# Kernel tuning notes

Measured on AMD Instinct MI355X. Metric: run time of the kernel, lower is better.

The kernel has to match this reference:

```python
import jax, jax.numpy as jnp
import numpy as np

N_ORDER = 256
PRED_LEN = 192
SEQ_LEN = 768
ENC_IN = 21
BATCH = 16
MULTISCALE = [1, 2, 4]
MODES = 32  # min(32, min(pred_len, seq_len)//2)


def _transition(N):
    Q = np.arange(N, dtype=np.float64)
    R = (2 * Q + 1)[:, None]
    j, i = np.meshgrid(Q, Q)
    A = np.where(i < j, -1, (-1.0) ** (i - j + 1)) * R
    B = (-1.0) ** Q[:, None] * R
    return A, B


def _bilinear(A, B, dt):
    # scipy cont2discrete(method='bilinear'): Ad=(I-dt/2 A)^-1 (I+dt/2 A), Bd=(I-dt/2 A)^-1 dt B
    N = A.shape[0]
    I = np.eye(N)
    ima = I - (dt / 2.0) * A
    Ad = np.linalg.solve(ima, I + (dt / 2.0) * A)
    Bd = np.linalg.solve(ima, dt * B)
    return Ad, Bd.squeeze(-1)


def _legendre_eval(N, x):
    # Legendre P_n(x) via three-term recurrence; returns [len(x), N]
    T = x.shape[0]
    P = np.zeros((N, T))
    P[0] = 1.0
    if N > 1:
        P[1] = x
    for n in range(2, N):
        P[n] = ((2 * n - 1) * x * P[n - 1] - (n - 1) * P[n - 2]) / n
    return P.T


def setup_inputs() -> dict:
    key = jax.random.key(0)
    ks = jax.random.split(key, 12)
    inp = {"x_enc": jax.random.normal(ks[0], (BATCH, SEQ_LEN, ENC_IN), dtype=jnp.float32)}
    Ac, Bc = _transition(N_ORDER)
    scale = 1.0 / (N_ORDER * N_ORDER)
    for idx, m in enumerate(MULTISCALE):
        dt = 1.0 / PRED_LEN / m
        Ad, Bd = _bilinear(Ac, Bc, dt)
        vals = np.arange(0.0, 1.0, dt)
        E = _legendre_eval(N_ORDER, 1.0 - 2.0 * vals)
        inp[f"A{idx}"] = jnp.asarray(Ad, jnp.float32)
        inp[f"B{idx}"] = jnp.asarray(Bd, jnp.float32)
        inp[f"E{idx}"] = jnp.asarray(E, jnp.float32)
        inp[f"Wr{idx}"] = scale * jax.random.uniform(ks[1 + 2 * idx], (N_ORDER, N_ORDER, MODES), dtype=jnp.float32)
        inp[f"Wi{idx}"] = scale * jax.random.uniform(ks[2 + 2 * idx], (N_ORDER, N_ORDER, MODES), dtype=jnp.float32)
    inp["mlp_w"] = 0.1 * jax.random.normal(ks[10], (1, len(MULTISCALE)), dtype=jnp.float32)
    inp["mlp_b"] = jnp.zeros((1,), jnp.float32)
    return inp


def _hippo(x, A, Bv):
    # x: [B, E, L]; c_t = c_{t-1} @ A^T + f_t * B  (F.linear(c, A) == c @ A.T)
    def step(c, f):
        c = c @ A.T + f[..., None] * Bv
        return c, c
    c0 = jnp.zeros(x.shape[:-1] + (A.shape[0],), x.dtype)
    _, cs = jax.lax.scan(step, c0, jnp.moveaxis(x, -1, 0))
    return jnp.moveaxis(cs, 0, -1)  # [B, E, N, L]


def _spec_conv(x, Wr, Wi):
    # x: [B, E, N_in, L]; keep first MODES rfft modes, complex channel mix, irfft
    L = x.shape[-1]
    a = jnp.fft.rfft(x, axis=-1)[..., :MODES]
    W = (Wr + 1j * Wi).astype(jnp.complex64)
    out = jnp.einsum('bjix,iox->bjox', a, W)
    nf = L // 2 + 1
    out_full = jnp.pad(out, ((0, 0), (0, 0), (0, 0), (0, nf - MODES)))
    return jnp.fft.irfft(out_full, n=L, axis=-1)


def reference(x_enc, A0, B0, E0, Wr0, Wi0, A1, B1, E1, Wr1, Wi1, A2, B2, E2, Wr2, Wi2, mlp_w, mlp_b):
    params = [(A0, B0, E0, Wr0, Wi0), (A1, B1, E1, Wr1, Wi1), (A2, B2, E2, Wr2, Wi2)]
    x_decs = []
    for m, (A, Bv, E, Wr, Wi) in zip(MULTISCALE, params):
        x_in = x_enc[:, -m * PRED_LEN:]                      # [B, L, E]
        c = _hippo(jnp.transpose(x_in, (0, 2, 1)), A, Bv)    # [B, E, N, L]
        out1 = _spec_conv(c, Wr, Wi)                         # [B, E, N, L]
        x_dec_c = out1[:, :, :, PRED_LEN - 1]                # seq_len >= pred_len, jump_dist=0
        x_decs.append(x_dec_c @ E[-PRED_LEN:].T)             # [B, E, pred_len]
    x_dec = jnp.stack(x_decs, axis=-1)                       # [B, E, pred_len, 3]
    out = x_dec @ mlp_w[0] + mlp_b[0]                        # Linear(3,1) then squeeze
    return jnp.transpose(out, (0, 2, 1))                     # [B, pred_len, E]
```

## Files before the change

kernel.cpp:

```cpp
#include <hip/hip_runtime.h>
#include <math.h>

#define PI_F 3.14159265358979323846f

#define W_OFF    0
#define AP_OFF   344064
#define KT_OFF   737280
#define KTOT_OFF 995328
#define Y_OFF    1142784
#define S_OFF    1142784
#define F_OFF    1732608
#define QT_OFF   10579968
#define WS_FLOATS 27095040

__device__ __forceinline__ int off_w_f(int s)  { return 49152  * ((1 << s) - 1); }
__device__ __forceinline__ int qoff_f(int s)   { return 2359296 * ((1 << s) - 1); }
__device__ __forceinline__ int ktoff_f(int s)  { return 36864  * ((1 << s) - 1); }
__device__ __forceinline__ int foff_f(int s)   { return 1179648 * ((1 << s) - 1); }

template<bool BT>
__device__ __forceinline__ void gemm_tile(const float* __restrict__ A,
                                          const float* __restrict__ B,
                                          float* __restrict__ C,
                                          int M, int N, int ldc, int m0, int n0)
{
    __shared__ float As[16][68];
    __shared__ float Bs[16][68];
    const int tid = threadIdx.x;
    const int tx = tid & 15;
    const int ty = tid >> 4;
    const int r  = tid >> 2;
    const int kq = (tid & 3) << 2;

    float acc[4][4] = {{0.f,0.f,0.f,0.f},{0.f,0.f,0.f,0.f},
                       {0.f,0.f,0.f,0.f},{0.f,0.f,0.f,0.f}};

    for (int kk = 0; kk < 256; kk += 16) {
        float4 av = make_float4(0.f, 0.f, 0.f, 0.f);
        if (m0 + r < M)
            av = *(const float4*)(A + (size_t)(m0 + r) * 256 + kk + kq);
        As[kq + 0][r] = av.x; As[kq + 1][r] = av.y;
        As[kq + 2][r] = av.z; As[kq + 3][r] = av.w;

        if (BT) {
            float4 bv = make_float4(0.f, 0.f, 0.f, 0.f);
            if (n0 + r < N)
                bv = *(const float4*)(B + (size_t)(n0 + r) * 256 + kk + kq);
            Bs[kq + 0][r] = bv.x; Bs[kq + 1][r] = bv.y;
            Bs[kq + 2][r] = bv.z; Bs[kq + 3][r] = bv.w;
        } else {
            const int kb = tid >> 4;
            const int j4 = (tid & 15) << 2;
            float4 bv = *(const float4*)(B + (size_t)(kk + kb) * 256 + n0 + j4);
            *(float4*)(&Bs[kb][j4]) = bv;
        }
        __syncthreads();

        #pragma unroll
        for (int k = 0; k < 16; ++k) {
            float4 a4 = *(const float4*)(&As[k][ty << 2]);
            float4 b4 = *(const float4*)(&Bs[k][tx << 2]);
            acc[0][0] = fmaf(a4.x, b4.x, acc[0][0]);
            acc[0][1] = fmaf(a4.x, b4.y, acc[0][1]);
            acc[0][2] = fmaf(a4.x, b4.z, acc[0][2]);
            acc[0][3] = fmaf(a4.x, b4.w, acc[0][3]);
            acc[1][0] = fmaf(a4.y, b4.x, acc[1][0]);
            acc[1][1] = fmaf(a4.y, b4.y, acc[1][1]);
            acc[1][2] = fmaf(a4.y, b4.z, acc[1][2]);
            acc[1][3] = fmaf(a4.y, b4.w, acc[1][3]);
            acc[2][0] = fmaf(a4.z, b4.x, acc[2][0]);
            acc[2][1] = fmaf(a4.z, b4.y, acc[2][1]);
            acc[2][2] = fmaf(a4.z, b4.z, acc[2][2]);
            acc[2][3] = fmaf(a4.z, b4.w, acc[2][3]);
            acc[3][0] = fmaf(a4.w, b4.x, acc[3][0]);
            acc[3][1] = fmaf(a4.w, b4.y, acc[3][1]);
            acc[3][2] = fmaf(a4.w, b4.z, acc[3][2]);
            acc[3][3] = fmaf(a4.w, b4.w, acc[3][3]);
        }
        __syncthreads();
    }

    #pragma unroll
    for (int u = 0; u < 4; ++u) {
        int row = m0 + (ty << 2) + u;
        if (row < M) {
            float4 cv = make_float4(acc[u][0], acc[u][1], acc[u][2], acc[u][3]);
            *(float4*)(C + (size_t)row * ldc + n0 + (tx << 2)) = cv;
        }
    }
}

__device__ __forceinline__ void gemm64x128(const float* __restrict__ A,
                                           const float* __restrict__ B,
                                           float* __restrict__ C, int ldc)
{
    __shared__ float As[16][68];
    __shared__ float Bs[16][132];

    const int tid = threadIdx.x;
    const int tx = tid & 15;
    const int ty = tid >> 4;
    const int ra  = tid >> 2;
    const int kqa = (tid & 3) << 2;
    const int rb  = tid >> 1;
    const int kq8 = (tid & 1) << 3;

    float acc[2][4][4];
    #pragma unroll
    for (int g = 0; g < 2; ++g)
        #pragma unroll
        for (int u = 0; u < 4; ++u)
            #pragma unroll
            for (int v = 0; v < 4; ++v) acc[g][u][v] = 0.f;

    for (int kk = 0; kk < 256; kk += 16) {
        float4 av = *(const float4*)(A + (size_t)ra * 256 + kk + kqa);
        As[kqa + 0][ra] = av.x; As[kqa + 1][ra] = av.y;
        As[kqa + 2][ra] = av.z; As[kqa + 3][ra] = av.w;

        const float* bp = B + (size_t)rb * 256 + kk + kq8;
        float4 b0 = *(const float4*)(bp);
        float4 b1 = *(const float4*)(bp + 4);
        Bs[kq8 + 0][rb] = b0.x; Bs[kq8 + 1][rb] = b0.y;
        Bs[kq8 + 2][rb] = b0.z; Bs[kq8 + 3][rb] = b0.w;
        Bs[kq8 + 4][rb] = b1.x; Bs[kq8 + 5][rb] = b1.y;
        Bs[kq8 + 6][rb] = b1.z; Bs[kq8 + 7][rb] = b1.w;
        __syncthreads();

        #pragma unroll
        for (int kq = 0; kq < 16; ++kq) {
            float4 a  = *(const float4*)(&As[kq][4 * ty]);
            float4 b0v = *(const float4*)(&Bs[kq][4 * tx]);
            float4 b1v = *(const float4*)(&Bs[kq][4 * tx + 64]);
            float af[4] = {a.x, a.y, a.z, a.w};
            float bf[8] = {b0v.x, b0v.y, b0v.z, b0v.w, b1v.x, b1v.y, b1v.z, b1v.w};
            #pragma unroll
            for (int g = 0; g < 2; ++g)
                #pragma unroll
                for (int u = 0; u < 4; ++u)
                    #pragma unroll
                    for (int v = 0; v < 4; ++v)
                        acc[g][u][v] = fmaf(af[u], bf[g * 4 + v], acc[g][u][v]);
        }
        __syncthreads();
    }

    #pragma unroll
    for (int u = 0; u < 4; ++u) {
        int row = 4 * ty + u;
        #pragma unroll
        for (int g = 0; g < 2; ++g) {
            float4 cv = make_float4(acc[g][u][0], acc[g][u][1],
                                    acc[g][u][2], acc[g][u][3]);
            *(float4*)(C + (size_t)row * ldc + 4 * tx + 64 * g) = cv;
        }
    }
}

__global__ void k_init(const float* B0, const float* B1, const float* B2, float* ws)
{
    int s = blockIdx.x;
    const float* Bv = (s == 0) ? B0 : (s == 1) ? B1 : B2;
    ws[W_OFF + off_w_f(s) + threadIdx.x] = Bv[threadIdx.x];
}

__global__ void k_level(int n, const float* A0, const float* A1, const float* A2,
                        float* ws)
{
    int s = blockIdx.z;
    int L = 192 << s;
    const float* Ain = (s == 0) ? A0 : (s == 1) ? A1 : A2;
    float* wbase = ws + W_OFF + off_w_f(s);
    float* bufA  = ws + AP_OFF + s * 131072;
    float* bufB  = bufA + 65536;
    const float* src = (n == 0) ? Ain : (((n - 1) & 1) ? bufB : bufA);

    int y = blockIdx.y;
    if (y < 4) {
        int p2 = 1 << n;
        if (p2 >= L) return;
        int cnt = min(p2, L - p2);
        int m0 = y * 64;
        if (m0 >= cnt) return;
        gemm_tile<true>(wbase, src, wbase + (size_t)p2 * 256,
                        cnt, 256, 256, m0, blockIdx.x * 64);
    } else {
        if ((2 << n) >= L) return;
        float* dst = (n & 1) ? bufB : bufA;
        gemm_tile<false>(src, src, dst, 256, 256, 256, (y - 4) * 64, blockIdx.x * 64);
    }
}

__global__ void k_transpose(const float* Wr0, const float* Wi0,
                            const float* Wr1, const float* Wi1,
                            const float* Wr2, const float* Wi2, float* ws)
{
    int bid = blockIdx.x;
    int i  = bid & 255;
    int ri = (bid >> 8) & 1;
    int s  = bid >> 9;
    const float* W;
    if (s == 0)      W = ri ? Wi0 : Wr0;
    else if (s == 1) W = ri ? Wi1 : Wr1;
    else             W = ri ? Wi2 : Wr2;

    int o = threadIdx.x;
    int sri = s * 2 + ri;
    const float* Wrow = W + (size_t)i * 8192 + (size_t)o * 32;
    #pragma unroll
    for (int k = 0; k < 32; ++k) {
        ws[QT_OFF + ((size_t)(sri * 32 + k) * 256 + i) * 256 + o] = Wrow[k];
    }
}

__global__ void __launch_bounds__(256, 4)
k_gemm_Y4(const float* E0, const float* E1, const float* E2, float* __restrict__ ws)
{
    const int s  = blockIdx.z;
    const int L  = 192 << s;
    const int zz = blockIdx.x >> 1;
    const int n0 = (blockIdx.x & 1) * 128;
    const int z  = s * 64 + zz;
    const int m0 = blockIdx.y * 64;
    const float* E = (s == 0) ? E0 : (s == 1) ? E1 : E2;

    const float* Ap = E + (size_t)(L - 192) * 256 + (size_t)m0 * 256;
    const float* Bp = ws + QT_OFF + (size_t)z * 65536 + (size_t)n0 * 256;
    float* Cp = ws + Y_OFF + (size_t)z * 49152 + (size_t)m0 * 256 + n0;
    gemm64x128(Ap, Bp, Cp, 256);
}

__global__ void __launch_bounds__(256, 4)
k_gemm_Q4(float* __restrict__ ws)
{
    const int y = blockIdx.y;
    int s, yt;
    if (y < 3)      { s = 0; yt = y; }
    else if (y < 9) { s = 1; yt = y - 3; }
    else            { s = 2; yt = y - 9; }
    const int m0 = yt * 64;
    const int n0 = blockIdx.x * 128;

    const float* Ap = ws + W_OFF + off_w_f(s) + (size_t)m0 * 256;
    const float* Bp = ws + Y_OFF + (size_t)s * 3145728 + (size_t)n0 * 256;
    float* Cp = ws + QT_OFF + qoff_f(s) + (size_t)m0 * 12288 + n0;
    gemm64x128(Ap, Bp, Cp, 12288);
}

__global__ void k_scanA(float* __restrict__ ws)
{
    const int c = blockIdx.x;
    const int k = blockIdx.y;
    const int s = blockIdx.z;
    const int L = 192 << s;
    const int C = L >> 4;
    const int p = threadIdx.x;

    __shared__ float twc[768], tws[768];
    for (int m = p; m < L; m += 192) {
        float ang = -2.f * PI_F * (float)m / (float)L;
        float ss, cc; sincosf(ang, &ss, &cc);
        twc[m] = cc; tws[m] = ss;
    }
    __syncthreads();

    const float* Qr = ws + QT_OFF + qoff_f(s) + (size_t)k * 192;
    const float* Qi = Qr + 6144;

    float ar = 0.f, ai = 0.f;
    const int d0 = c * C;
    int ph = (k * d0) % L;
    for (int j = 0; j < C; ++j) {
        int d = d0 + j;
        float qr = Qr[(size_t)d * 12288 + p];
        float qi = Qi[(size_t)d * 12288 + p];
        float cc = twc[ph], sn = tws[ph];
        ar = fmaf(cc, qr, fmaf(-sn, qi, ar));
        ai = fmaf(cc, qi, fmaf( sn, qr, ai));
        ph += k; if (ph >= L) ph -= L;
    }
    size_t sb = (size_t)((s * 32 + k) * 16 + c) * 384;
    ws[S_OFF + sb + p]       = ar;
    ws[S_OFF + sb + 192 + p] = ai;
}

__global__ void k_scanB(float* __restrict__ ws)
{
    const int c = blockIdx.x;
    const int k = blockIdx.y;
    const int s = blockIdx.z;
    const int L = 192 << s;
    const int C = L >> 4;
    const int p = threadIdx.x;

    __shared__ float twc[768], tws[768];
    for (int m = p; m < L; m += 192) {
        float ang = -2.f * PI_F * (float)m / (float)L;
        float ss, cc; sincosf(ang, &ss, &cc);
        twc[m] = cc; tws[m] = ss;
    }
    __syncthreads();

    float ar = 0.f, ai = 0.f;
    size_t sbase = (size_t)(s * 32 + k) * 16 * 384;
    for (int c2 = 0; c2 < c; ++c2) {
        ar += ws[S_OFF + sbase + (size_t)c2 * 384 + p];
        ai += ws[S_OFF + sbase + (size_t)c2 * 384 + 192 + p];
    }

    const float ck = ((k == 0) ? 1.f : 2.f) / (float)L;
    const float* Qr = ws + QT_OFF + qoff_f(s) + (size_t)k * 192;
    const float* Qi = Qr + 6144;
    float* F = ws + F_OFF + foff_f(s);

    const int d0 = c * C;
    int ph = (k * d0) % L;
    int m1 = d0 + 192 - L; if (m1 < 0) m1 += L;
    int ph2 = (k * m1) % L;
    for (int j = 0; j < C; ++j) {
        int d = d0 + j;
        float qr = Qr[(size_t)d * 12288 + p];
        float qi = Qi[(size_t)d * 12288 + p];
        float cc = twc[ph], sn = tws[ph];
        ar = fmaf(cc, qr, fmaf(-sn, qi, ar));
        ai = fmaf(cc, qi, fmaf( sn, qr, ai));
        float f = ck * fmaf(twc[ph2], ar, tws[ph2] * ai);
        int sidx = L - 1 - d;
        F[((size_t)sidx * 32 + k) * 192 + p] = f;
        ph  += k; if (ph  >= L) ph  -= L;
        ph2 += k; if (ph2 >= L) ph2 -= L;
    }
}

__global__ void k_kred(float* __restrict__ ws)
{
    int bid = blockIdx.x;
    int s, sidx;
    if (bid < 192)      { s = 0; sidx = bid; }
    else if (bid < 576) { s = 1; sidx = bid - 192; }
    else                { s = 2; sidx = bid - 576; }
    int p = threadIdx.x;
    const float* F = ws + F_OFF + foff_f(s) + (size_t)sidx * 32 * 192;
    float sum = 0.f;
    #pragma unroll
    for (int k = 0; k < 32; ++k)
        sum += F[k * 192 + p];
    ws[KT_OFF + ktoff_f(s) + (size_t)sidx * 192 + p] = sum;
}

__global__ void k_combine(float* ws, const float* mw)
{
    int idx = blockIdx.x * 256 + threadIdx.x;
    if (idx >= 147456) return;
    int tau = idx / 192;
    int p   = idx - tau * 192;
    float sum = 0.f;
    #pragma unroll
    for (int s = 0; s < 3; ++s) {
        int L = 192 << s;
        int off = 768 - L;
        if (tau >= off)
            sum = fmaf(mw[s], ws[KT_OFF + ktoff_f(s) + (size_t)(tau - off) * 192 + p], sum);
    }
    ws[KTOT_OFF + idx] = sum;
}

__global__ void k_out(const float* __restrict__ x, const float* __restrict__ ws,
                      const float* __restrict__ mb, float* __restrict__ out)
{
    int bid = blockIdx.x;
    int b = bid / 21;
    int c = bid - b * 21;
    __shared__ float xl[768];
    for (int t = threadIdx.x; t < 768; t += 192)
        xl[t] = x[((size_t)b * 768 + t) * 21 + c];
    __syncthreads();

    int p = threadIdx.x;
    const float* K = ws + KTOT_OFF;
    float acc = 0.f;
    for (int tau = 0; tau < 768; ++tau)
        acc = fmaf(xl[tau], K[(size_t)tau * 192 + p], acc);
    out[((size_t)b * 192 + p) * 21 + c] = acc + mb[0];
}

extern "C" void kernel_launch(void* const* d_in, const int* in_sizes, int n_in,
                              void* d_out, int out_size, void* d_ws, size_t ws_size,
                              hipStream_t stream)
{
    const float* x   = (const float*)d_in[0];
    const float* A0  = (const float*)d_in[1];
    const float* B0  = (const float*)d_in[2];
    const float* E0  = (const float*)d_in[3];
    const float* Wr0 = (const float*)d_in[4];
    const float* Wi0 = (const float*)d_in[5];
    const float* A1  = (const float*)d_in[6];
    const float* B1  = (const float*)d_in[7];
    const float* E1  = (const float*)d_in[8];
    const float* Wr1 = (const float*)d_in[9];
    const float* Wi1 = (const float*)d_in[10];
    const float* A2  = (const float*)d_in[11];
    const float* B2  = (const float*)d_in[12];
    const float* E2  = (const float*)d_in[13];
    const float* Wr2 = (const float*)d_in[14];
    const float* Wi2 = (const float*)d_in[15];
    const float* mw  = (const float*)d_in[16];
    const float* mb  = (const float*)d_in[17];
    float* ws  = (float*)d_ws;
    float* out = (float*)d_out;

    if (ws_size < (size_t)WS_FLOATS * sizeof(float)) {
        hipMemsetAsync(d_out, 0, (size_t)out_size * sizeof(float), stream);
        return;
    }

    k_init<<<3, 256, 0, stream>>>(B0, B1, B2, ws);
    for (int n = 0; n < 10; ++n)
        k_level<<<dim3(4, 8, 3), 256, 0, stream>>>(n, A0, A1, A2, ws);
    k_transpose<<<1536, 256, 0, stream>>>(Wr0, Wi0, Wr1, Wi1, Wr2, Wi2, ws);
    k_gemm_Y4<<<dim3(128, 3, 3), 256, 0, stream>>>(E0, E1, E2, ws);
    k_gemm_Q4<<<dim3(96, 21), 256, 0, stream>>>(ws);
    k_scanA<<<dim3(16, 32, 3), 192, 0, stream>>>(ws);
    k_scanB<<<dim3(16, 32, 3), 192, 0, stream>>>(ws);
    k_kred<<<1344, 192, 0, stream>>>(ws);
    k_combine<<<576, 256, 0, stream>>>(ws, mw);
    k_out<<<336, 192, 0, stream>>>(x, ws, mb, out);
}
```

Before: 471.4 us.

## Double-buffer GEMM shared tiles and stage weight transpose through LDS

The 64x128 GEMM now uses two shared-memory buffers. The next K-slice is loaded from global memory into registers while the current slice is computed, which cuts one barrier per iteration and hides load latency. The weight transpose kernel now reads each 8192-float slab with coalesced float4 loads into a padded shared tile, then writes the transposed output, replacing the strided 32-float-per-thread reads. Doubling shared memory in the GEMM may lower occupancy, and the prefetch raises register pressure.

```diff
diff --git a/kernel.cpp b/kernel.cpp
--- a/kernel.cpp
+++ b/kernel.cpp
@@ -94,8 +94,8 @@
                                            const float* __restrict__ B,
                                            float* __restrict__ C, int ldc)
 {
-    __shared__ float As[16][68];
-    __shared__ float Bs[16][132];
+    __shared__ float As[2][16][68];
+    __shared__ float Bs[2][16][132];
 
     const int tid = threadIdx.x;
     const int tx = tid & 15;
@@ -113,25 +113,37 @@
             #pragma unroll
             for (int v = 0; v < 4; ++v) acc[g][u][v] = 0.f;
 
-    for (int kk = 0; kk < 256; kk += 16) {
-        float4 av = *(const float4*)(A + (size_t)ra * 256 + kk + kqa);
-        As[kqa + 0][ra] = av.x; As[kqa + 1][ra] = av.y;
-        As[kqa + 2][ra] = av.z; As[kqa + 3][ra] = av.w;
-
-        const float* bp = B + (size_t)rb * 256 + kk + kq8;
+    {
+        float4 av = *(const float4*)(A + (size_t)ra * 256 + kqa);
+        As[0][kqa + 0][ra] = av.x; As[0][kqa + 1][ra] = av.y;
+        As[0][kqa + 2][ra] = av.z; As[0][kqa + 3][ra] = av.w;
+        const float* bp = B + (size_t)rb * 256 + kq8;
         float4 b0 = *(const float4*)(bp);
         float4 b1 = *(const float4*)(bp + 4);
-        Bs[kq8 + 0][rb] = b0.x; Bs[kq8 + 1][rb] = b0.y;
-        Bs[kq8 + 2][rb] = b0.z; Bs[kq8 + 3][rb] = b0.w;
-        Bs[kq8 + 4][rb] = b1.x; Bs[kq8 + 5][rb] = b1.y;
-        Bs[kq8 + 6][rb] = b1.z; Bs[kq8 + 7][rb] = b1.w;
+        Bs[0][kq8 + 0][rb] = b0.x; Bs[0][kq8 + 1][rb] = b0.y;
+        Bs[0][kq8 + 2][rb] = b0.z; Bs[0][kq8 + 3][rb] = b0.w;
+        Bs[0][kq8 + 4][rb] = b1.x; Bs[0][kq8 + 5][rb] = b1.y;
+        Bs[0][kq8 + 6][rb] = b1.z; Bs[0][kq8 + 7][rb] = b1.w;
+    }
+
+    for (int kk = 0; kk < 16; ++kk) {
+        const int cur = kk & 1;
+        float4 av = make_float4(0.f, 0.f, 0.f, 0.f);
+        float4 b0 = av, b1 = av;
+        if (kk < 15) {
+            const int ko = (kk + 1) << 4;
+            av = *(const float4*)(A + (size_t)ra * 256 + ko + kqa);
+            const float* bp = B + (size_t)rb * 256 + ko + kq8;
+            b0 = *(const float4*)(bp);
+            b1 = *(const float4*)(bp + 4);
+        }
         __syncthreads();
 
         #pragma unroll
         for (int kq = 0; kq < 16; ++kq) {
-            float4 a  = *(const float4*)(&As[kq][4 * ty]);
-            float4 b0v = *(const float4*)(&Bs[kq][4 * tx]);
-            float4 b1v = *(const float4*)(&Bs[kq][4 * tx + 64]);
+            float4 a   = *(const float4*)(&As[cur][kq][4 * ty]);
+            float4 b0v = *(const float4*)(&Bs[cur][kq][4 * tx]);
+            float4 b1v = *(const float4*)(&Bs[cur][kq][4 * tx + 64]);
             float af[4] = {a.x, a.y, a.z, a.w};
             float bf[8] = {b0v.x, b0v.y, b0v.z, b0v.w, b1v.x, b1v.y, b1v.z, b1v.w};
             #pragma unroll
@@ -142,7 +154,16 @@
                     for (int v = 0; v < 4; ++v)
                         acc[g][u][v] = fmaf(af[u], bf[g * 4 + v], acc[g][u][v]);
         }
-        __syncthreads();
+
+        if (kk < 15) {
+            const int nxt = cur ^ 1;
+            As[nxt][kqa + 0][ra] = av.x; As[nxt][kqa + 1][ra] = av.y;
+            As[nxt][kqa + 2][ra] = av.z; As[nxt][kqa + 3][ra] = av.w;
+            Bs[nxt][kq8 + 0][rb] = b0.x; Bs[nxt][kq8 + 1][rb] = b0.y;
+            Bs[nxt][kq8 + 2][rb] = b0.z; Bs[nxt][kq8 + 3][rb] = b0.w;
+            Bs[nxt][kq8 + 4][rb] = b1.x; Bs[nxt][kq8 + 5][rb] = b1.y;
+            Bs[nxt][kq8 + 6][rb] = b1.z; Bs[nxt][kq8 + 7][rb] = b1.w;
+        }
     }
 
     #pragma unroll
@@ -195,6 +216,7 @@
                             const float* Wr1, const float* Wi1,
                             const float* Wr2, const float* Wi2, float* ws)
 {
+    __shared__ float t[256][33];
     int bid = blockIdx.x;
     int i  = bid & 255;
     int ri = (bid >> 8) & 1;
@@ -204,12 +226,23 @@
     else if (s == 1) W = ri ? Wi1 : Wr1;
     else             W = ri ? Wi2 : Wr2;
 
-    int o = threadIdx.x;
+    const int tid = threadIdx.x;
+    const float* slab = W + (size_t)i * 8192;
+    #pragma unroll
+    for (int j = 0; j < 8; ++j) {
+        int f = j * 1024 + tid * 4;
+        float4 v = *(const float4*)(slab + f);
+        int o = f >> 5;
+        int k = f & 31;
+        t[o][k + 0] = v.x; t[o][k + 1] = v.y;
+        t[o][k + 2] = v.z; t[o][k + 3] = v.w;
+    }
+    __syncthreads();
+
     int sri = s * 2 + ri;
-    const float* Wrow = W + (size_t)i * 8192 + (size_t)o * 32;
     #pragma unroll
     for (int k = 0; k < 32; ++k) {
-        ws[QT_OFF + ((size_t)(sri * 32 + k) * 256 + i) * 256 + o] = Wrow[k];
+        ws[QT_OFF + (size_t)(sri * 32 + k) * 65536 + (size_t)i * 256 + tid] = t[tid][k];
     }
 }
 
```

Measured after the change: 426.0 us. -9.6%, faster.

## Use 128-thread GEMM blocks with 8x8 microtiles and LDS-staged weight transpose

Applied to the files above, without the earlier changes.

The 64x128 GEMM now runs with 128 threads, each computing an 8x8 register tile (two 4-row halves by two 4-column groups), so the shared-memory loads are amortised over more FMAs. Global loads are rearranged to match: each thread loads 8 A elements and 16 B elements per k-step. The weight transpose kernel now reads each 8192-float slab with coalesced float4 loads into a padded LDS tile and writes out coalesced, replacing strided scalar reads. This raises register pressure per thread and halves the thread count per block, which may reduce latency hiding.

```diff
diff --git a/kernel.cpp b/kernel.cpp
--- a/kernel.cpp
+++ b/kernel.cpp
@@ -98,63 +98,75 @@
     __shared__ float Bs[16][132];
 
     const int tid = threadIdx.x;
-    const int tx = tid & 15;
-    const int ty = tid >> 4;
-    const int ra  = tid >> 2;
-    const int kqa = (tid & 3) << 2;
-    const int rb  = tid >> 1;
+    const int tx  = tid & 15;
+    const int ty  = tid >> 4;
+    const int ra  = tid >> 1;
     const int kq8 = (tid & 1) << 3;
 
-    float acc[2][4][4];
-    #pragma unroll
-    for (int g = 0; g < 2; ++g)
+    float acc[2][2][4][4];
+    #pragma unroll
+    for (int h = 0; h < 2; ++h)
         #pragma unroll
-        for (int u = 0; u < 4; ++u)
+        for (int g = 0; g < 2; ++g)
             #pragma unroll
-            for (int v = 0; v < 4; ++v) acc[g][u][v] = 0.f;
+            for (int u = 0; u < 4; ++u)
+                #pragma unroll
+                for (int v = 0; v < 4; ++v) acc[h][g][u][v] = 0.f;
 
     for (int kk = 0; kk < 256; kk += 16) {
-        float4 av = *(const float4*)(A + (size_t)ra * 256 + kk + kqa);
-        As[kqa + 0][ra] = av.x; As[kqa + 1][ra] = av.y;
-        As[kqa + 2][ra] = av.z; As[kqa + 3][ra] = av.w;
-
-        const float* bp = B + (size_t)rb * 256 + kk + kq8;
+        const float* ap = A + (size_t)ra * 256 + kk + kq8;
+        float4 a0 = *(const float4*)(ap);
+        float4 a1 = *(const float4*)(ap + 4);
+        As[kq8 + 0][ra] = a0.x; As[kq8 + 1][ra] = a0.y;
+        As[kq8 + 2][ra] = a0.z; As[kq8 + 3][ra] = a0.w;
+        As[kq8 + 4][ra] = a1.x; As[kq8 + 5][ra] = a1.y;
+        As[kq8 + 6][ra] = a1.z; As[kq8 + 7][ra] = a1.w;
+
+        const float* bp = B + (size_t)tid * 256 + kk;
         float4 b0 = *(const float4*)(bp);
         float4 b1 = *(const float4*)(bp + 4);
-        Bs[kq8 + 0][rb] = b0.x; Bs[kq8 + 1][rb] = b0.y;
-        Bs[kq8 + 2][rb] = b0.z; Bs[kq8 + 3][rb] = b0.w;
-        Bs[kq8 + 4][rb] = b1.x; Bs[kq8 + 5][rb] = b1.y;
-        Bs[kq8 + 6][rb] = b1.z; Bs[kq8 + 7][rb] = b1.w;
+        float4 b2 = *(const float4*)(bp + 8);
+        float4 b3 = *(const float4*)(bp + 12);
+        Bs[ 0][tid] = b0.x; Bs[ 1][tid] = b0.y; Bs[ 2][tid] = b0.z; Bs[ 3][tid] = b0.w;
+        Bs[ 4][tid] = b1.x; Bs[ 5][tid] = b1.y; Bs[ 6][tid] = b1.z; Bs[ 7][tid] = b1.w;
+        Bs[ 8][tid] = b2.x; Bs[ 9][tid] = b2.y; Bs[10][tid] = b2.z; Bs[11][tid] = b2.w;
+        Bs[12][tid] = b3.x; Bs[13][tid] = b3.y; Bs[14][tid] = b3.z; Bs[15][tid] = b3.w;
         __syncthreads();
 
         #pragma unroll
         for (int kq = 0; kq < 16; ++kq) {
-            float4 a  = *(const float4*)(&As[kq][4 * ty]);
-            float4 b0v = *(const float4*)(&Bs[kq][4 * tx]);
-            float4 b1v = *(const float4*)(&Bs[kq][4 * tx + 64]);
-            float af[4] = {a.x, a.y, a.z, a.w};
-            float bf[8] = {b0v.x, b0v.y, b0v.z, b0v.w, b1v.x, b1v.y, b1v.z, b1v.w};
+            float4 aA = *(const float4*)(&As[kq][4 * ty]);
+            float4 aB = *(const float4*)(&As[kq][4 * ty + 32]);
+            float4 bA = *(const float4*)(&Bs[kq][4 * tx]);
+            float4 bB = *(const float4*)(&Bs[kq][4 * tx + 64]);
+            float af[8] = {aA.x, aA.y, aA.z, aA.w, aB.x, aB.y, aB.z, aB.w};
+            float bf[8] = {bA.x, bA.y, bA.z, bA.w, bB.x, bB.y, bB.z, bB.w};
             #pragma unroll
-            for (int g = 0; g < 2; ++g)
+            for (int h = 0; h < 2; ++h)
                 #pragma unroll
                 for (int u = 0; u < 4; ++u)
                     #pragma unroll
-                    for (int v = 0; v < 4; ++v)
-                        acc[g][u][v] = fmaf(af[u], bf[g * 4 + v], acc[g][u][v]);
+                    for (int g = 0; g < 2; ++g)
+                        #pragma unroll
+                        for (int v = 0; v < 4; ++v)
+                            acc[h][g][u][v] = fmaf(af[h * 4 + u], bf[g * 4 + v],
+                                                   acc[h][g][u][v]);
         }
         __syncthreads();
     }
 
     #pragma unroll
-    for (int u = 0; u < 4; ++u) {
-        int row = 4 * ty + u;
+    for (int h = 0; h < 2; ++h)
         #pragma unroll
-        for (int g = 0; g < 2; ++g) {
-            float4 cv = make_float4(acc[g][u][0], acc[g][u][1],
-                                    acc[g][u][2], acc[g][u][3]);
-            *(float4*)(C + (size_t)row * ldc + 4 * tx + 64 * g) = cv;
+        for (int u = 0; u < 4; ++u) {
+            int row = 4 * ty + 32 * h + u;
+            #pragma unroll
+            for (int g = 0; g < 2; ++g) {
+                float4 cv = make_float4(acc[h][g][u][0], acc[h][g][u][1],
+                                        acc[h][g][u][2], acc[h][g][u][3]);
+                *(float4*)(C + (size_t)row * ldc + 4 * tx + 64 * g) = cv;
+            }
         }
-    }
 }
 
 __global__ void k_init(const float* B0, const float* B1, const float* B2, float* ws)
@@ -195,6 +207,7 @@
                             const float* Wr1, const float* Wi1,
                             const float* Wr2, const float* Wi2, float* ws)
 {
+    __shared__ float t[256][33];
     int bid = blockIdx.x;
     int i  = bid & 255;
     int ri = (bid >> 8) & 1;
@@ -204,16 +217,27 @@
     else if (s == 1) W = ri ? Wi1 : Wr1;
     else             W = ri ? Wi2 : Wr2;
 
-    int o = threadIdx.x;
+    const int tid = threadIdx.x;
+    const float* slab = W + (size_t)i * 8192;
+    #pragma unroll
+    for (int j = 0; j < 8; ++j) {
+        int f = j * 1024 + tid * 4;
+        float4 v = *(const float4*)(slab + f);
+        int o = f >> 5;
+        int k = f & 31;
+        t[o][k + 0] = v.x; t[o][k + 1] = v.y;
+        t[o][k + 2] = v.z; t[o][k + 3] = v.w;
+    }
+    __syncthreads();
+
     int sri = s * 2 + ri;
-    const float* Wrow = W + (size_t)i * 8192 + (size_t)o * 32;
     #pragma unroll
     for (int k = 0; k < 32; ++k) {
-        ws[QT_OFF + ((size_t)(sri * 32 + k) * 256 + i) * 256 + o] = Wrow[k];
-    }
-}
-
-__global__ void __launch_bounds__(256, 4)
+        ws[QT_OFF + (size_t)(sri * 32 + k) * 65536 + (size_t)i * 256 + tid] = t[tid][k];
+    }
+}
+
+__global__ void __launch_bounds__(128, 4)
 k_gemm_Y4(const float* E0, const float* E1, const float* E2, float* __restrict__ ws)
 {
     const int s  = blockIdx.z;
@@ -230,7 +254,7 @@
     gemm64x128(Ap, Bp, Cp, 256);
 }
 
-__global__ void __launch_bounds__(256, 4)
+__global__ void __launch_bounds__(128, 4)
 k_gemm_Q4(float* __restrict__ ws)
 {
     const int y = blockIdx.y;
@@ -418,8 +442,8 @@
     for (int n = 0; n < 10; ++n)
         k_level<<<dim3(4, 8, 3), 256, 0, stream>>>(n, A0, A1, A2, ws);
     k_transpose<<<1536, 256, 0, stream>>>(Wr0, Wi0, Wr1, Wi1, Wr2, Wi2, ws);
-    k_gemm_Y4<<<dim3(128, 3, 3), 256, 0, stream>>>(E0, E1, E2, ws);
-    k_gemm_Q4<<<dim3(96, 21), 256, 0, stream>>>(ws);
+    k_gemm_Y4<<<dim3(128, 3, 3), 128, 0, stream>>>(E0, E1, E2, ws);
+    k_gemm_Q4<<<dim3(96, 21), 128, 0, stream>>>(ws);
     k_scanA<<<dim3(16, 32, 3), 192, 0, stream>>>(ws);
     k_scanB<<<dim3(16, 32, 3), 192, 0, stream>>>(ws);
     k_kred<<<1344, 192, 0, stream>>>(ws);
```

New measurement: 429.0 us. 1.1x faster.
